# Kernel tuning notes

Measured on AMD Instinct MI355X. Metric: run time of the kernel, lower is better.

The kernel has to match this reference:

```python
import jax, jax.numpy as jnp
import numpy as np

STEP_SIZE = 0.01
ITERATION = 1.0
F_FORCING = 8.0
N_STEPS = int(round(ITERATION / STEP_SIZE))  # 100 fixed RK4 steps

BATCH = 8192
INPUT_SIZE = 784
SYSTEM_COUNT = 1024
OUTPUT_SIZE = 10


def setup_inputs() -> dict:
    key = jax.random.key(0)
    k_x, k_w1, k_b1, k_w2, k_b2 = jax.random.split(key, 5)
    x = jax.random.normal(k_x, (BATCH, INPUT_SIZE), dtype=jnp.float32)
    # nn.Linear-style params (out_features, in_features)
    s1 = 1.0 / np.sqrt(INPUT_SIZE)
    W1 = jax.random.uniform(k_w1, (SYSTEM_COUNT, INPUT_SIZE), jnp.float32, -s1, s1)
    b1 = jax.random.uniform(k_b1, (SYSTEM_COUNT,), jnp.float32, -s1, s1)
    s2 = 1.0 / np.sqrt(SYSTEM_COUNT)
    W2 = jax.random.uniform(k_w2, (OUTPUT_SIZE, SYSTEM_COUNT), jnp.float32, -s2, s2)
    b2 = jax.random.uniform(k_b2, (OUTPUT_SIZE,), jnp.float32, -s2, s2)
    return {"x": x, "W1": W1, "b1": b1, "W2": W2, "b2": b2}


def _lorenz96(x):
    # (roll(x,-1) - roll(x,2)) * roll(x,1) - x + F   along feature dim 1
    return (jnp.roll(x, -1, axis=1) - jnp.roll(x, 2, axis=1)) * jnp.roll(x, 1, axis=1) - x + F_FORCING


def _rk4_integrate(x0):
    h = jnp.float32(STEP_SIZE)

    def step(x, _):
        k1 = _lorenz96(x)
        k2 = _lorenz96(x + 0.5 * h * k1)
        k3 = _lorenz96(x + 0.5 * h * k2)
        k4 = _lorenz96(x + h * k3)
        x_next = x + (h / 6.0) * (k1 + 2.0 * k2 + 2.0 * k3 + k4)
        return x_next, None

    xT, _ = jax.lax.scan(step, x0, None, length=N_STEPS)
    return xT


def reference(x, W1, b1, W2, b2):
    h = x @ W1.T + b1                 # [B, systemCount]
    h = _rk4_integrate(h)             # RK4 over [0, iteration], step 0.01
    logits = h @ W2.T + b2            # [B, output_size]
    return jax.nn.log_softmax(logits, axis=1)
```

## Files before the change

### kernel.cpp

```cpp
#include <hip/hip_runtime.h>
#include <hip/hip_bf16.h>
#include <math.h>

#define BATCH 8192
#define INSZ 784
#define SYS 1024
#define OUTSZ 10
#define NSTEP 100
#define HSTEP 0.01f
#define FFORCE 8.0f

typedef short short8 __attribute__((ext_vector_type(8)));
typedef float float4v __attribute__((ext_vector_type(4)));
typedef float v2f __attribute__((ext_vector_type(2)));

static __device__ __forceinline__ short f2bf(float x) {
    __hip_bfloat16 b = __float2bfloat16(x);
    return __builtin_bit_cast(short, b);
}
static __device__ __forceinline__ float bf2f(short s) {
    unsigned int u = ((unsigned int)(unsigned short)s) << 16;
    return __builtin_bit_cast(float, u);
}

static __device__ __forceinline__ v2f pkfma(v2f a, v2f b, v2f c) {
    return __builtin_elementwise_fma(a, b, c);
}
static __device__ __forceinline__ v2f mk2(float x, float y) {
    v2f r; r.x = x; r.y = y; return r;
}
static __device__ __forceinline__ v2f swp(v2f v) {
    return __builtin_shufflevector(v, v, 1, 0);
}
static __device__ __forceinline__ v2f sh2(v2f v, int ln) {
    v2f r; r.x = __shfl(v.x, ln); r.y = __shfl(v.y, ln); return r;
}

#define BMg 128
#define BNg 128
#define BKg 32
#define LDK 40

__global__ __launch_bounds__(256, 3) void gemm1_kernel(
    const float* __restrict__ x, const float* __restrict__ W1,
    const float* __restrict__ b1, float* __restrict__ h)
{
    __shared__ short Ah[BMg * LDK], Al[BMg * LDK];
    __shared__ short Bh[BNg * LDK], Bl[BNg * LDK];

    const int t  = threadIdx.x;
    const int bm = blockIdx.y * BMg;
    const int bn = blockIdx.x * BNg;

    const int srow = t >> 1;
    const int kq   = (t & 1) * 16;

    const int wv   = t >> 6;
    const int lane = t & 63;
    const int lm   = lane & 15;
    const int q    = lane >> 4;
    const int rb   = (wv & 1) * 64;
    const int cb   = (wv >> 1) * 64;

    float4v acc[4][4];
    #pragma unroll
    for (int i = 0; i < 4; ++i)
        #pragma unroll
        for (int j = 0; j < 4; ++j) {
            acc[i][j][0] = 0.f; acc[i][j][1] = 0.f;
            acc[i][j][2] = 0.f; acc[i][j][3] = 0.f;
        }

    const float* xa0 = x  + (size_t)(bm + srow) * INSZ + kq;
    const float* wb0 = W1 + (size_t)(bn + srow) * INSZ + kq;

    for (int it = 0; it < 25; ++it) {
        const int k0 = it * BKg;
        {
            const bool valid = (k0 + kq) < INSZ;
            float va[16], vb[16];
            if (valid) {
                #pragma unroll
                for (int p = 0; p < 4; ++p) {
                    float4 xv = ((const float4*)(xa0 + k0))[p];
                    float4 bv = ((const float4*)(wb0 + k0))[p];
                    va[4*p+0] = xv.x; va[4*p+1] = xv.y; va[4*p+2] = xv.z; va[4*p+3] = xv.w;
                    vb[4*p+0] = bv.x; vb[4*p+1] = bv.y; vb[4*p+2] = bv.z; vb[4*p+3] = bv.w;
                }
            } else {
                #pragma unroll
                for (int j = 0; j < 16; ++j) { va[j] = 0.f; vb[j] = 0.f; }
            }
            short8 ahi[2], alo[2], bhi[2], blo[2];
            #pragma unroll
            for (int j = 0; j < 16; ++j) {
                short h1 = f2bf(va[j]);
                short l1 = f2bf(va[j] - bf2f(h1));
                short h2 = f2bf(vb[j]);
                short l2 = f2bf(vb[j] - bf2f(h2));
                ahi[j >> 3][j & 7] = h1;  alo[j >> 3][j & 7] = l1;
                bhi[j >> 3][j & 7] = h2;  blo[j >> 3][j & 7] = l2;
            }
            const int base = srow * LDK + kq;
            *(short8*)&Ah[base] = ahi[0];  *(short8*)&Ah[base + 8] = ahi[1];
            *(short8*)&Al[base] = alo[0];  *(short8*)&Al[base + 8] = alo[1];
            *(short8*)&Bh[base] = bhi[0];  *(short8*)&Bh[base + 8] = bhi[1];
            *(short8*)&Bl[base] = blo[0];  *(short8*)&Bl[base + 8] = blo[1];
        }
        __syncthreads();

        short8 bhf[4], blf[4];
        #pragma unroll
        for (int fj = 0; fj < 4; ++fj) {
            const int off = (cb + fj * 16 + lm) * LDK + q * 8;
            bhf[fj] = *(const short8*)&Bh[off];
            blf[fj] = *(const short8*)&Bl[off];
        }
        #pragma unroll
        for (int fi = 0; fi < 4; ++fi) {
            const int off = (rb + fi * 16 + lm) * LDK + q * 8;
            short8 ah = *(const short8*)&Ah[off];
            short8 al = *(const short8*)&Al[off];
            #pragma unroll
            for (int fj = 0; fj < 4; ++fj) {
                acc[fi][fj] = __builtin_amdgcn_mfma_f32_16x16x32_bf16(ah, bhf[fj], acc[fi][fj], 0, 0, 0);
                acc[fi][fj] = __builtin_amdgcn_mfma_f32_16x16x32_bf16(ah, blf[fj], acc[fi][fj], 0, 0, 0);
                acc[fi][fj] = __builtin_amdgcn_mfma_f32_16x16x32_bf16(al, bhf[fj], acc[fi][fj], 0, 0, 0);
            }
        }
        __syncthreads();
    }

    #pragma unroll
    for (int fj = 0; fj < 4; ++fj) {
        const int col  = bn + cb + fj * 16 + lm;
        const float bias = b1[col];
        #pragma unroll
        for (int fi = 0; fi < 4; ++fi) {
            const int row0 = bm + rb + fi * 16 + q * 4;
            #pragma unroll
            for (int r = 0; r < 4; ++r)
                h[(size_t)(row0 + r) * SYS + col] = acc[fi][fj][r] + bias;
        }
    }
}

__global__ __launch_bounds__(256, 4) void rk4_kernel(
    const float* __restrict__ hbuf, const float* __restrict__ W2,
    const float* __restrict__ b2, float* __restrict__ out)
{
    const int lane = threadIdx.x & 63;
    const int w    = threadIdx.x >> 6;
    const int row  = blockIdx.x * 4 + w;

    const int laneL = (lane + 63) & 63;
    const int laneR = (lane + 1) & 63;
    const bool atL  = (lane == 0);
    const bool atR  = (lane == 63);

    v2f X[8];
    {
        const float4* b4 = (const float4*)(hbuf + (size_t)row * SYS);
        float4 a0 = b4[lane * 2], a1 = b4[lane * 2 + 1];
        float4 c0 = b4[128 + lane * 2], c1 = b4[129 + lane * 2];
        X[0] = mk2(a0.x, c0.x); X[1] = mk2(a0.y, c0.y);
        X[2] = mk2(a0.z, c0.z); X[3] = mk2(a0.w, c0.w);
        X[4] = mk2(a1.x, c1.x); X[5] = mk2(a1.y, c1.y);
        X[6] = mk2(a1.z, c1.z); X[7] = mk2(a1.w, c1.w);
    }

    const v2f Fv = mk2(FFORCE, FFORCE);
    v2f acc[8], T[8];

    auto deriv_ip = [&](v2f (&y)[8]) {
        v2f r1 = sh2(y[0], laneR);  r1 = atR ? swp(r1) : r1;
        v2f l1 = sh2(y[7], laneL);  l1 = atL ? swp(l1) : l1;
        v2f l2 = sh2(y[6], laneL);  l2 = atL ? swp(l2) : l2;
        v2f p2 = l2, p1 = l1, cur = y[0];
        #pragma unroll
        for (int i = 0; i < 8; ++i) {
            v2f yp1 = (i < 7) ? y[i + 1] : r1;
            v2f nv  = pkfma(yp1 - p2, p1, Fv - cur);
            p2 = p1; p1 = cur;
            if (i < 7) cur = y[i + 1];
            y[i] = nv;
        }
    };

    const v2f c_half = mk2(0.5f * HSTEP, 0.5f * HSTEP);
    const v2f c_full = mk2(HSTEP, HSTEP);
    const v2f c_two  = mk2(2.0f, 2.0f);
    const v2f c_six  = mk2(HSTEP / 6.0f, HSTEP / 6.0f);

    #pragma unroll 1
    for (int s = 0; s < NSTEP; ++s) {
        {
            v2f r1 = sh2(X[0], laneR);  r1 = atR ? swp(r1) : r1;
            v2f l1 = sh2(X[7], laneL);  l1 = atL ? swp(l1) : l1;
            v2f l2 = sh2(X[6], laneL);  l2 = atL ? swp(l2) : l2;
            #pragma unroll
            for (int i = 0; i < 8; ++i) {
                v2f yp1 = (i < 7) ? X[i + 1] : r1;
                v2f ym1 = (i > 0) ? X[i - 1] : l1;
                v2f ym2 = (i > 1) ? X[i - 2] : ((i == 1) ? l1 : l2);
                acc[i] = pkfma(yp1 - ym2, ym1, Fv - X[i]);
            }
        }
        #pragma unroll
        for (int i = 0; i < 8; ++i) T[i] = pkfma(c_half, acc[i], X[i]);
        deriv_ip(T);
        #pragma unroll
        for (int i = 0; i < 8; ++i) {
            acc[i] = pkfma(c_two, T[i], acc[i]);
            T[i]   = pkfma(c_half, T[i], X[i]);
        }
        deriv_ip(T);
        #pragma unroll
        for (int i = 0; i < 8; ++i) {
            acc[i] = pkfma(c_two, T[i], acc[i]);
            T[i]   = pkfma(c_full, T[i], X[i]);
        }
        deriv_ip(T);
        #pragma unroll
        for (int i = 0; i < 8; ++i)
            X[i] = pkfma(c_six, acc[i] + T[i], X[i]);
    }

    float l[OUTSZ];
    #pragma unroll
    for (int o = 0; o < OUTSZ; ++o) {
        const float4* w4 = (const float4*)(W2 + (size_t)o * SYS);
        float4 wa0 = w4[lane * 2], wa1 = w4[lane * 2 + 1];
        float4 wc0 = w4[128 + lane * 2], wc1 = w4[129 + lane * 2];
        v2f s2 = mk2(0.f, 0.f);
        s2 = pkfma(X[0], mk2(wa0.x, wc0.x), s2);
        s2 = pkfma(X[1], mk2(wa0.y, wc0.y), s2);
        s2 = pkfma(X[2], mk2(wa0.z, wc0.z), s2);
        s2 = pkfma(X[3], mk2(wa0.w, wc0.w), s2);
        s2 = pkfma(X[4], mk2(wa1.x, wc1.x), s2);
        s2 = pkfma(X[5], mk2(wa1.y, wc1.y), s2);
        s2 = pkfma(X[6], mk2(wa1.z, wc1.z), s2);
        s2 = pkfma(X[7], mk2(wa1.w, wc1.w), s2);
        float s = s2.x + s2.y;
        #pragma unroll
        for (int dlt = 1; dlt < 64; dlt <<= 1) s += __shfl_xor(s, dlt);
        l[o] = s + b2[o];
    }

    float m = l[0];
    #pragma unroll
    for (int o = 1; o < OUTSZ; ++o) m = fmaxf(m, l[o]);
    float ssum = 0.f;
    #pragma unroll
    for (int o = 0; o < OUTSZ; ++o) ssum += __expf(l[o] - m);
    const float lse = m + __logf(ssum);

    float v = l[0] - lse;
    #pragma unroll
    for (int o = 1; o < OUTSZ; ++o)
        if (lane == o) v = l[o] - lse;
    if (lane < OUTSZ)
        out[(size_t)row * OUTSZ + lane] = v;
}

extern "C" void kernel_launch(void* const* d_in, const int* in_sizes, int n_in,
                              void* d_out, int out_size, void* d_ws, size_t ws_size,
                              hipStream_t stream)
{
    const float* x  = (const float*)d_in[0];
    const float* W1 = (const float*)d_in[1];
    const float* b1 = (const float*)d_in[2];
    const float* W2 = (const float*)d_in[3];
    const float* b2 = (const float*)d_in[4];
    float* out = (float*)d_out;
    float* h   = (float*)d_ws;

    dim3 g1(SYS / BNg, BATCH / BMg);
    gemm1_kernel<<<g1, 256, 0, stream>>>(x, W1, b1, h);

    rk4_kernel<<<BATCH / 4, 256, 0, stream>>>(h, W2, b2, out);
}
```

Before: 454.7 us.

## Pack two batch rows per wavefront in RK4 packed-FMA lanes

Each wavefront now integrates two batch rows at once. The packed v2f lanes hold the same feature index from two rows, where before they held two halves of one row, and each lane owns 16 contiguous features. This removes the per-shuffle lane swap fixups at the wavefront edges, since neighbour wrap is now purely cross-lane within a row, and it amortises the shuffles over twice the work. Register pressure doubles per thread (16-element arrays), which may reduce occupancy under launch_bounds(256,4), and the grid halves to 1024 blocks.

```diff
diff --git a/kernel.cpp b/kernel.cpp
--- a/kernel.cpp
+++ b/kernel.cpp
@@ -28,9 +28,6 @@
 }
 static __device__ __forceinline__ v2f mk2(float x, float y) {
     v2f r; r.x = x; r.y = y; return r;
-}
-static __device__ __forceinline__ v2f swp(v2f v) {
-    return __builtin_shufflevector(v, v, 1, 0);
 }
 static __device__ __forceinline__ v2f sh2(v2f v, int ln) {
     v2f r; r.x = __shfl(v.x, ln); r.y = __shfl(v.y, ln); return r;
@@ -151,38 +148,40 @@
 {
     const int lane = threadIdx.x & 63;
     const int w    = threadIdx.x >> 6;
-    const int row  = blockIdx.x * 4 + w;
+    const int rowA = blockIdx.x * 8 + w * 2;
+    const int rowB = rowA + 1;
 
     const int laneL = (lane + 63) & 63;
     const int laneR = (lane + 1) & 63;
-    const bool atL  = (lane == 0);
-    const bool atR  = (lane == 63);
-
-    v2f X[8];
+
+    v2f X[16];
     {
-        const float4* b4 = (const float4*)(hbuf + (size_t)row * SYS);
-        float4 a0 = b4[lane * 2], a1 = b4[lane * 2 + 1];
-        float4 c0 = b4[128 + lane * 2], c1 = b4[129 + lane * 2];
-        X[0] = mk2(a0.x, c0.x); X[1] = mk2(a0.y, c0.y);
-        X[2] = mk2(a0.z, c0.z); X[3] = mk2(a0.w, c0.w);
-        X[4] = mk2(a1.x, c1.x); X[5] = mk2(a1.y, c1.y);
-        X[6] = mk2(a1.z, c1.z); X[7] = mk2(a1.w, c1.w);
+        const float4* a4 = (const float4*)(hbuf + (size_t)rowA * SYS) + lane * 4;
+        const float4* b4 = (const float4*)(hbuf + (size_t)rowB * SYS) + lane * 4;
+        #pragma unroll
+        for (int k = 0; k < 4; ++k) {
+            float4 av = a4[k], bv = b4[k];
+            X[4*k+0] = mk2(av.x, bv.x);
+            X[4*k+1] = mk2(av.y, bv.y);
+            X[4*k+2] = mk2(av.z, bv.z);
+            X[4*k+3] = mk2(av.w, bv.w);
+        }
     }
 
     const v2f Fv = mk2(FFORCE, FFORCE);
-    v2f acc[8], T[8];
-
-    auto deriv_ip = [&](v2f (&y)[8]) {
-        v2f r1 = sh2(y[0], laneR);  r1 = atR ? swp(r1) : r1;
-        v2f l1 = sh2(y[7], laneL);  l1 = atL ? swp(l1) : l1;
-        v2f l2 = sh2(y[6], laneL);  l2 = atL ? swp(l2) : l2;
+    v2f acc[16], T[16];
+
+    auto deriv_ip = [&](v2f (&y)[16]) {
+        v2f r1 = sh2(y[0],  laneR);
+        v2f l1 = sh2(y[15], laneL);
+        v2f l2 = sh2(y[14], laneL);
         v2f p2 = l2, p1 = l1, cur = y[0];
         #pragma unroll
-        for (int i = 0; i < 8; ++i) {
-            v2f yp1 = (i < 7) ? y[i + 1] : r1;
+        for (int i = 0; i < 16; ++i) {
+            v2f yp1 = (i < 15) ? y[i + 1] : r1;
             v2f nv  = pkfma(yp1 - p2, p1, Fv - cur);
             p2 = p1; p1 = cur;
-            if (i < 7) cur = y[i + 1];
+            if (i < 15) cur = y[i + 1];
             y[i] = nv;
         }
     };
@@ -195,72 +194,80 @@
     #pragma unroll 1
     for (int s = 0; s < NSTEP; ++s) {
         {
-            v2f r1 = sh2(X[0], laneR);  r1 = atR ? swp(r1) : r1;
-            v2f l1 = sh2(X[7], laneL);  l1 = atL ? swp(l1) : l1;
-            v2f l2 = sh2(X[6], laneL);  l2 = atL ? swp(l2) : l2;
-            #pragma unroll
-            for (int i = 0; i < 8; ++i) {
-                v2f yp1 = (i < 7) ? X[i + 1] : r1;
-                v2f ym1 = (i > 0) ? X[i - 1] : l1;
-                v2f ym2 = (i > 1) ? X[i - 2] : ((i == 1) ? l1 : l2);
+            v2f r1 = sh2(X[0],  laneR);
+            v2f l1 = sh2(X[15], laneL);
+            v2f l2 = sh2(X[14], laneL);
+            #pragma unroll
+            for (int i = 0; i < 16; ++i) {
+                v2f yp1 = (i < 15) ? X[i + 1] : r1;
+                v2f ym1 = (i > 0)  ? X[i - 1] : l1;
+                v2f ym2 = (i > 1)  ? X[i - 2] : ((i == 1) ? l1 : l2);
                 acc[i] = pkfma(yp1 - ym2, ym1, Fv - X[i]);
             }
         }
         #pragma unroll
-        for (int i = 0; i < 8; ++i) T[i] = pkfma(c_half, acc[i], X[i]);
+        for (int i = 0; i < 16; ++i) T[i] = pkfma(c_half, acc[i], X[i]);
         deriv_ip(T);
         #pragma unroll
-        for (int i = 0; i < 8; ++i) {
+        for (int i = 0; i < 16; ++i) {
             acc[i] = pkfma(c_two, T[i], acc[i]);
             T[i]   = pkfma(c_half, T[i], X[i]);
         }
         deriv_ip(T);
         #pragma unroll
-        for (int i = 0; i < 8; ++i) {
+        for (int i = 0; i < 16; ++i) {
             acc[i] = pkfma(c_two, T[i], acc[i]);
             T[i]   = pkfma(c_full, T[i], X[i]);
         }
         deriv_ip(T);
         #pragma unroll
-        for (int i = 0; i < 8; ++i)
+        for (int i = 0; i < 16; ++i)
             X[i] = pkfma(c_six, acc[i] + T[i], X[i]);
     }
 
-    float l[OUTSZ];
+    v2f l[OUTSZ];
     #pragma unroll
     for (int o = 0; o < OUTSZ; ++o) {
-        const float4* w4 = (const float4*)(W2 + (size_t)o * SYS);
-        float4 wa0 = w4[lane * 2], wa1 = w4[lane * 2 + 1];
-        float4 wc0 = w4[128 + lane * 2], wc1 = w4[129 + lane * 2];
+        const float4* w4 = (const float4*)(W2 + (size_t)o * SYS) + lane * 4;
         v2f s2 = mk2(0.f, 0.f);
-        s2 = pkfma(X[0], mk2(wa0.x, wc0.x), s2);
-        s2 = pkfma(X[1], mk2(wa0.y, wc0.y), s2);
-        s2 = pkfma(X[2], mk2(wa0.z, wc0.z), s2);
-        s2 = pkfma(X[3], mk2(wa0.w, wc0.w), s2);
-        s2 = pkfma(X[4], mk2(wa1.x, wc1.x), s2);
-        s2 = pkfma(X[5], mk2(wa1.y, wc1.y), s2);
-        s2 = pkfma(X[6], mk2(wa1.z, wc1.z), s2);
-        s2 = pkfma(X[7], mk2(wa1.w, wc1.w), s2);
-        float s = s2.x + s2.y;
-        #pragma unroll
-        for (int dlt = 1; dlt < 64; dlt <<= 1) s += __shfl_xor(s, dlt);
-        l[o] = s + b2[o];
-    }
-
-    float m = l[0];
-    #pragma unroll
-    for (int o = 1; o < OUTSZ; ++o) m = fmaxf(m, l[o]);
-    float ssum = 0.f;
-    #pragma unroll
-    for (int o = 0; o < OUTSZ; ++o) ssum += __expf(l[o] - m);
-    const float lse = m + __logf(ssum);
-
-    float v = l[0] - lse;
-    #pragma unroll
-    for (int o = 1; o < OUTSZ; ++o)
-        if (lane == o) v = l[o] - lse;
-    if (lane < OUTSZ)
-        out[(size_t)row * OUTSZ + lane] = v;
+        #pragma unroll
+        for (int k = 0; k < 4; ++k) {
+            float4 wv = w4[k];
+            s2 = pkfma(X[4*k+0], mk2(wv.x, wv.x), s2);
+            s2 = pkfma(X[4*k+1], mk2(wv.y, wv.y), s2);
+            s2 = pkfma(X[4*k+2], mk2(wv.z, wv.z), s2);
+            s2 = pkfma(X[4*k+3], mk2(wv.w, wv.w), s2);
+        }
+        #pragma unroll
+        for (int dlt = 1; dlt < 64; dlt <<= 1) {
+            s2.x += __shfl_xor(s2.x, dlt);
+            s2.y += __shfl_xor(s2.y, dlt);
+        }
+        const float bo = b2[o];
+        l[o] = s2 + mk2(bo, bo);
+    }
+
+    v2f m = l[0];
+    #pragma unroll
+    for (int o = 1; o < OUTSZ; ++o) m = __builtin_elementwise_max(m, l[o]);
+    v2f ssum = mk2(0.f, 0.f);
+    #pragma unroll
+    for (int o = 0; o < OUTSZ; ++o) {
+        v2f d = l[o] - m;
+        ssum = ssum + mk2(__expf(d.x), __expf(d.y));
+    }
+    const v2f lse = m + mk2(__logf(ssum.x), __logf(ssum.y));
+
+    float vA = l[0].x - lse.x;
+    float vB = l[0].y - lse.y;
+    #pragma unroll
+    for (int o = 1; o < OUTSZ; ++o) {
+        if (lane == o) { vA = l[o].x - lse.x; vB = l[o].y - lse.y; }
+    }
+    if (lane < OUTSZ) {
+        out[(size_t)rowA * OUTSZ + lane] = vA;
+        out[(size_t)rowB * OUTSZ + lane] = vB;
+    }
 }
 
 extern "C" void kernel_launch(void* const* d_in, const int* in_sizes, int n_in,
@@ -278,5 +285,5 @@
     dim3 g1(SYS / BNg, BATCH / BMg);
     gemm1_kernel<<<g1, 256, 0, stream>>>(x, W1, b1, h);
 
-    rk4_kernel<<<BATCH / 4, 256, 0, stream>>>(h, W2, b2, out);
-}
+    rk4_kernel<<<BATCH / 8, 256, 0, stream>>>(h, W2, b2, out);
+}
```

After: 431.4 us. 1.05x faster.
